# Kernel tuning notes

Measured on AMD Instinct MI355X. Metric: run time of the kernel, lower is better.

Reference implementation:

```python
import jax, jax.numpy as jnp
import numpy as np

VOCAB = 21128
D_WENLAN = 2048
SENT_LEN = 44  # hard-coded in original forward


def setup_inputs() -> dict:
    key = jax.random.key(0)
    ks = jax.random.split(key, 8)
    B, S, P = 32, 8, 32
    L = S * SENT_LEN  # 352
    concat_output = jax.random.normal(ks[0], (B, S, D_WENLAN), jnp.float32)
    input_ids = jax.random.randint(ks[1], (B, L), 0, VOCAB, jnp.int32)
    topic_ids = jax.random.randint(ks[2], (B, P), 0, VOCAB, jnp.int32)
    tpw_att_mask = jnp.ones((B, P), jnp.int32)
    tpw_type_ids = jnp.zeros((B, P), jnp.int32)
    attention_mask = jnp.ones((B, L), jnp.int32)
    type_ids = jax.random.randint(ks[3], (B, L), 0, 8, jnp.int32)
    token_table = jax.random.normal(ks[4], (VOCAB, D_WENLAN), jnp.float32) * 0.02
    W1 = jax.random.normal(ks[5], (D_WENLAN, 512), jnp.float32) * 0.02
    b1 = jnp.zeros((512,), jnp.float32)
    W2 = jax.random.normal(ks[6], (512, 768), jnp.float32) * 0.02
    b2 = jnp.zeros((768,), jnp.float32)
    return dict(concat_output=concat_output, input_ids=input_ids, topic_ids=topic_ids,
                tpw_att_mask=tpw_att_mask, tpw_type_ids=tpw_type_ids,
                attention_mask=attention_mask, type_ids=type_ids,
                token_table=token_table, W1=W1, b1=b1, W2=W2, b2=b2)


def reference(concat_output, input_ids, topic_ids, tpw_att_mask, tpw_type_ids,
              attention_mask, type_ids, token_table, W1, b1, W2, b2):
    B, S, D = concat_output.shape
    # vectorized replacement of the python double-loop dict lookups:
    topic_emb = token_table[topic_ids]                      # [B,P,2048]
    inp_emb = token_table[input_ids]                        # [B,L,2048]
    # scatter-add: each sentence block of 44 tokens gets its concat_output row added
    inp_emb = inp_emb.reshape(B, S, SENT_LEN, D) + concat_output[:, :, None, :]
    input_embs = jnp.concatenate([topic_emb, inp_emb.reshape(B, S * SENT_LEN, D)], axis=1)
    # projector MLP (Linear -> tanh -> Linear)
    h = jnp.tanh(jnp.einsum('btd,dk->btk', input_embs, W1) + b1)
    gpt_input_embs = jnp.einsum('btk,ke->bte', h, W2) + b2   # [B,P+L,768]
    # auxiliary concatenated tensors fed to gpt2 (is_train=True path)
    labels = jnp.concatenate([topic_ids, input_ids], axis=1)
    full_type_ids = jnp.concatenate([tpw_type_ids, type_ids], axis=1)
    full_att_mask = jnp.concatenate([tpw_att_mask, attention_mask], axis=1)
    return gpt_input_embs, labels, full_type_ids, full_att_mask
```

## Files before the change

### kernel.cpp

```cpp
#include <hip/hip_runtime.h>
#include <math.h>

typedef _Float16 half8 __attribute__((ext_vector_type(8)));
typedef float f32x4 __attribute__((ext_vector_type(4)));

#define BB 32
#define SS 8
#define PP 32
#define SENT 44
#define LL 352
#define TT 384
#define DD 2048
#define H1 512
#define H2 768
#define MM (BB*TT)
#define OUT0 (MM*H2)

#define GLL16(g, l) __builtin_amdgcn_global_load_lds( \
    (const __attribute__((address_space(1))) void*)(g), \
    (__attribute__((address_space(3))) void*)(l), 16, 0, 0)

__global__ __launch_bounds__(256) void transpose_f16_kernel(
    const float* __restrict__ src, _Float16* __restrict__ dst, int R, int C)
{
    __shared__ float tile[32][33];
    int c0 = blockIdx.x * 32;
    int r0 = blockIdx.y * 32;
    int tx = threadIdx.x & 31;
    int ty = threadIdx.x >> 5;
    #pragma unroll
    for (int i = 0; i < 4; ++i)
        tile[ty + i*8][tx] = src[(size_t)(r0 + ty + i*8) * C + c0 + tx];
    __syncthreads();
    #pragma unroll
    for (int i = 0; i < 4; ++i)
        dst[(size_t)(c0 + ty + i*8) * R + r0 + tx] = (_Float16)tile[tx][ty + i*8];
}

#define LOADA_T(S, ap, k0) {                                               \
    const float* _p = (ap) + (k0) + akq;                                   \
    float4 v0 = *(const float4*)(_p);                                      \
    float4 v1 = *(const float4*)(_p + 4);                                  \
    float4 v2 = *(const float4*)(_p + 8);                                  \
    float4 v3 = *(const float4*)(_p + 12);                                 \
    S[0]=v0.x; S[1]=v0.y; S[2]=v0.z; S[3]=v0.w;                            \
    S[4]=v1.x; S[5]=v1.y; S[6]=v1.z; S[7]=v1.w;                            \
    S[8]=v2.x; S[9]=v2.y; S[10]=v2.z; S[11]=v2.w;                          \
    S[12]=v3.x; S[13]=v3.y; S[14]=v3.z; S[15]=v3.w;                        \
}

#define WRITEA_T(S, dst) {                                                 \
    half8 h0, h1;                                                          \
    _Pragma("unroll")                                                      \
    for (int _j = 0; _j < 8; ++_j) { h0[_j] = (_Float16)S[_j];             \
                                     h1[_j] = (_Float16)S[8 + _j]; }       \
    *(half8*)&dst[(arow * 64 + akq) ^ aswz]     = h0;                      \
    *(half8*)&dst[(arow * 64 + akq + 8) ^ aswz] = h1;                      \
}

__global__ __launch_bounds__(256) void c1_kernel(
    const float*    __restrict__ concat_output,
    const _Float16* __restrict__ W1T,
    float*          __restrict__ C1)
{
    const int tid  = threadIdx.x;
    const int wid  = tid >> 6;
    const int lane = tid & 63;
    const int bm = blockIdx.x >> 2;
    const int bn = blockIdx.x & 3;

    __shared__ _Float16 As[2][64 * 64];
    __shared__ _Float16 Bs[2][128 * 64];

    const int arow = tid >> 2;
    const int akq  = (tid & 3) * 16;
    const int aswz = (arow & 7) << 3;
    const float* aptr = concat_output + (size_t)(bm * 64 + arow) * DD;

    const int rl = lane >> 3;
    const int cg = lane & 7;
    const _Float16* bsrc = W1T + (size_t)(bn * 128 + wid * 32 + rl) * DD
                               + ((cg ^ rl) << 3);

    #define C1B(buf, k0) {                                                \
        _Pragma("unroll")                                                 \
        for (int q = 0; q < 4; ++q)                                       \
            GLL16(bsrc + (size_t)q * 8 * DD + (k0),                       \
                  &Bs[buf][(wid * 4 + q) * 512]);                         \
    }

    const int wrow = (wid >> 1) * 32;
    const int wcol = (wid & 1) * 64;
    const int fr   = lane & 15;
    const int fg   = lane >> 4;

    f32x4 acc[2][4] = {};
    float a0[16], a1[16];

    C1B(0, 0);
    LOADA_T(a0, aptr, 0);
    LOADA_T(a1, aptr, 64);
    WRITEA_T(a0, As[0]);
    __syncthreads();

    #define C1_MFMA(buf) {                                                \
        _Pragma("unroll")                                                 \
        for (int kk = 0; kk < 2; ++kk) {                                  \
            half8 af[2], bf[4];                                           \
            _Pragma("unroll")                                             \
            for (int i = 0; i < 2; ++i) {                                 \
                int row = wrow + i * 16 + fr;                             \
                af[i] = *(const half8*)&As[buf][                          \
                    (row * 64 + kk * 32 + fg * 8) ^ ((row & 7) << 3)];    \
            }                                                             \
            _Pragma("unroll")                                             \
            for (int j = 0; j < 4; ++j) {                                 \
                int row = wcol + j * 16 + fr;                             \
                bf[j] = *(const half8*)&Bs[buf][                          \
                    (row * 64 + kk * 32 + fg * 8) ^ ((row & 7) << 3)];    \
            }                                                             \
            _Pragma("unroll")                                             \
            for (int i = 0; i < 2; ++i)                                   \
                _Pragma("unroll")                                         \
                for (int j = 0; j < 4; ++j)                               \
                    acc[i][j] = __builtin_amdgcn_mfma_f32_16x16x32_f16(   \
                        af[i], bf[j], acc[i][j], 0, 0, 0);                \
        }                                                                 \
    }

    for (int tt = 0; tt < 16; ++tt) {
        const int t2 = tt * 2;
        C1B(1, (t2 + 1) * 64);
        if (t2 + 2 < 32) LOADA_T(a0, aptr, (t2 + 2) * 64);
        C1_MFMA(0);
        WRITEA_T(a1, As[1]);
        __syncthreads();
        if (t2 + 2 < 32) C1B(0, (t2 + 2) * 64);
        if (t2 + 3 < 32) LOADA_T(a1, aptr, (t2 + 3) * 64);
        C1_MFMA(1);
        if (t2 + 2 < 32) WRITEA_T(a0, As[0]);
        __syncthreads();
    }

    #pragma unroll
    for (int i = 0; i < 2; ++i)
        #pragma unroll
        for (int j = 0; j < 4; ++j) {
            int col = bn * 128 + wcol + j * 16 + fr;
            #pragma unroll
            for (int r = 0; r < 4; ++r) {
                int row = bm * 64 + wrow + i * 16 + fg * 4 + r;
                C1[(size_t)row * H1 + col] = acc[i][j][r];
            }
        }
    #undef C1B
    #undef C1_MFMA
}

__global__ __launch_bounds__(256) void gemm1_kernel(
    const float*    __restrict__ token_table,
    const int*      __restrict__ topic_ids,
    const int*      __restrict__ input_ids,
    const _Float16* __restrict__ W1T,
    const float*    __restrict__ b1,
    const float*    __restrict__ C1,
    _Float16*       __restrict__ Hout)
{
    const int tid  = threadIdx.x;
    const int wid  = tid >> 6;
    const int lane = tid & 63;

    const int logical = ((blockIdx.x & 7) * 96) + (blockIdx.x >> 3);
    const int bm = logical >> 2;
    const int bn = logical & 3;

    __shared__ _Float16 As[2][64 * 64];
    __shared__ _Float16 Bs[2][128 * 64];

    const int arow = tid >> 2;
    const int akq  = (tid & 3) * 16;
    const int aswz = (arow & 7) << 3;

    const int m = bm * 64 + arow;
    const int b = m / TT;
    const int t = m % TT;
    const float* aptr;
    if (t < PP) {
        aptr = token_table + (size_t)topic_ids[b * PP + t] * DD;
    } else {
        aptr = token_table + (size_t)input_ids[b * LL + (t - PP)] * DD;
    }

    const int rl = lane >> 3;
    const int cg = lane & 7;
    const _Float16* bsrc = W1T + (size_t)(bn * 128 + wid * 32 + rl) * DD
                               + ((cg ^ rl) << 3);

    #define G1B(buf, k0) {                                                \
        _Pragma("unroll")                                                 \
        for (int q = 0; q < 4; ++q)                                       \
            GLL16(bsrc + (size_t)q * 8 * DD + (k0),                       \
                  &Bs[buf][(wid * 4 + q) * 512]);                         \
    }

    const int wrow = (wid >> 1) * 32;
    const int wcol = (wid & 1) * 64;
    const int fr   = lane & 15;
    const int fg   = lane >> 4;

    f32x4 acc[2][4] = {};
    float a0[16], a1[16];

    G1B(0, 0);
    LOADA_T(a0, aptr, 0);
    LOADA_T(a1, aptr, 64);
    WRITEA_T(a0, As[0]);
    __syncthreads();

    #define G1_MFMA(buf) {                                                \
        _Pragma("unroll")                                                 \
        for (int kk = 0; kk < 2; ++kk) {                                  \
            half8 af[2], bf[4];                                           \
            _Pragma("unroll")                                             \
            for (int i = 0; i < 2; ++i) {                                 \
                int row = wrow + i * 16 + fr;                             \
                af[i] = *(const half8*)&As[buf][                          \
                    (row * 64 + kk * 32 + fg * 8) ^ ((row & 7) << 3)];    \
            }                                                             \
            _Pragma("unroll")                                             \
            for (int j = 0; j < 4; ++j) {                                 \
                int row = wcol + j * 16 + fr;                             \
                bf[j] = *(const half8*)&Bs[buf][                          \
                    (row * 64 + kk * 32 + fg * 8) ^ ((row & 7) << 3)];    \
            }                                                             \
            _Pragma("unroll")                                             \
            for (int i = 0; i < 2; ++i)                                   \
                _Pragma("unroll")                                         \
                for (int j = 0; j < 4; ++j)                               \
                    acc[i][j] = __builtin_amdgcn_mfma_f32_16x16x32_f16(   \
                        af[i], bf[j], acc[i][j], 0, 0, 0);                \
        }                                                                 \
    }

    for (int tt = 0; tt < 16; ++tt) {
        const int t2 = tt * 2;
        G1B(1, (t2 + 1) * 64);
        if (t2 + 2 < 32) LOADA_T(a0, aptr, (t2 + 2) * 64);
        G1_MFMA(0);
        WRITEA_T(a1, As[1]);
        __syncthreads();
        if (t2 + 2 < 32) G1B(0, (t2 + 2) * 64);
        if (t2 + 3 < 32) LOADA_T(a1, aptr, (t2 + 3) * 64);
        G1_MFMA(1);
        if (t2 + 2 < 32) WRITEA_T(a0, As[0]);
        __syncthreads();
    }

    #pragma unroll
    for (int i = 0; i < 2; ++i) {
        #pragma unroll
        for (int j = 0; j < 4; ++j) {
            int col = bn * 128 + wcol + j * 16 + fr;
            float bias = b1[col];
            #pragma unroll
            for (int r = 0; r < 4; ++r) {
                int row = bm * 64 + wrow + i * 16 + fg * 4 + r;
                int rb = row / TT;
                int rt = row - rb * TT;
                float v = acc[i][j][r] + bias;
                if (rt >= PP)
                    v += C1[(size_t)(rb * SS + (rt - PP) / SENT) * H1 + col];
                Hout[(size_t)row * H1 + col] = (_Float16)tanhf(v);
            }
        }
    }
    #undef G1B
    #undef G1_MFMA
}

__global__ __launch_bounds__(256) void gemm2_kernel(
    const _Float16* __restrict__ Hin,
    const _Float16* __restrict__ W2T,
    const float*    __restrict__ b2,
    float*          __restrict__ out)
{
    const int tid  = threadIdx.x;
    const int wid  = tid >> 6;
    const int lane = tid & 63;

    const int logical = ((blockIdx.x & 7) * 64) + (blockIdx.x >> 3);
    const int bm = logical >> 2;
    const int bn = logical & 3;

    __shared__ _Float16 As[2][96 * 64];
    __shared__ _Float16 Bs[2][192 * 64];

    const int rl = lane >> 3;
    const int cg = lane & 7;
    const _Float16* asrc = Hin + (size_t)(bm * 96 + wid * 24 + rl) * H1
                               + ((cg ^ rl) << 3);
    const _Float16* bsrc = W2T + (size_t)(bn * 192 + wid * 48 + rl) * H1
                               + ((cg ^ rl) << 3);

    #define G2_ISSUE(buf, k0) {                                           \
        _Pragma("unroll")                                                 \
        for (int q = 0; q < 3; ++q)                                       \
            GLL16(asrc + (size_t)q * 8 * H1 + (k0),                       \
                  &As[buf][(wid * 3 + q) * 512]);                         \
        _Pragma("unroll")                                                 \
        for (int q = 0; q < 6; ++q)                                       \
            GLL16(bsrc + (size_t)q * 8 * H1 + (k0),                       \
                  &Bs[buf][(wid * 6 + q) * 512]);                         \
    }

    const int wrow = (wid >> 1) * 48;
    const int wcol = (wid & 1) * 96;
    const int fr   = lane & 15;
    const int fg   = lane >> 4;

    f32x4 acc[3][6] = {};

    G2_ISSUE(0, 0);

    const int NT = H1 / 64;
    for (int t = 0; t < NT; ++t) {
        __syncthreads();
        if (t + 1 < NT) G2_ISSUE((t + 1) & 1, (t + 1) * 64);
        const int cb = t & 1;
        #pragma unroll
        for (int kk = 0; kk < 2; ++kk) {
            half8 af[3], bf[6];
            #pragma unroll
            for (int i = 0; i < 3; ++i) {
                int row = wrow + i * 16 + fr;
                af[i] = *(const half8*)&As[cb][
                    (row * 64 + kk * 32 + fg * 8) ^ ((row & 7) << 3)];
            }
            #pragma unroll
            for (int j = 0; j < 6; ++j) {
                int row = wcol + j * 16 + fr;
                bf[j] = *(const half8*)&Bs[cb][
                    (row * 64 + kk * 32 + fg * 8) ^ ((row & 7) << 3)];
            }
            #pragma unroll
            for (int i = 0; i < 3; ++i)
                #pragma unroll
                for (int j = 0; j < 6; ++j)
                    acc[i][j] = __builtin_amdgcn_mfma_f32_16x16x32_f16(af[i], bf[j], acc[i][j], 0, 0, 0);
        }
    }

    #pragma unroll
    for (int i = 0; i < 3; ++i) {
        #pragma unroll
        for (int j = 0; j < 6; ++j) {
            int col = bn * 192 + wcol + j * 16 + fr;
            float bias = b2[col];
            #pragma unroll
            for (int r = 0; r < 4; ++r) {
                int row = bm * 96 + wrow + i * 16 + fg * 4 + r;
                out[(size_t)row * H2 + col] = acc[i][j][r] + bias;
            }
        }
    }
    #undef G2_ISSUE
}

__global__ __launch_bounds__(256) void aux_kernel(
    const int* __restrict__ topic_ids,
    const int* __restrict__ input_ids,
    const int* __restrict__ tpw_type_ids,
    const int* __restrict__ type_ids,
    const int* __restrict__ tpw_att_mask,
    const int* __restrict__ attention_mask,
    float* __restrict__ out)
{
    int idx = blockIdx.x * 256 + threadIdx.x;
    if (idx >= MM) return;
    int b = idx / TT, t = idx % TT;
    int lab, ty, mk;
    if (t < PP) {
        lab = topic_ids[b * PP + t];
        ty  = tpw_type_ids[b * PP + t];
        mk  = tpw_att_mask[b * PP + t];
    } else {
        int u = t - PP;
        lab = input_ids[b * LL + u];
        ty  = type_ids[b * LL + u];
        mk  = attention_mask[b * LL + u];
    }
    out[OUT0 + idx]          = (float)lab;
    out[OUT0 + MM + idx]     = (float)ty;
    out[OUT0 + 2 * MM + idx] = (float)mk;
}

extern "C" void kernel_launch(void* const* d_in, const int* in_sizes, int n_in,
                              void* d_out, int out_size, void* d_ws, size_t ws_size,
                              hipStream_t stream) {
    const float* concat_output  = (const float*)d_in[0];
    const int*   input_ids      = (const int*)d_in[1];
    const int*   topic_ids      = (const int*)d_in[2];
    const int*   tpw_att_mask   = (const int*)d_in[3];
    const int*   tpw_type_ids   = (const int*)d_in[4];
    const int*   attention_mask = (const int*)d_in[5];
    const int*   type_ids       = (const int*)d_in[6];
    const float* token_table    = (const float*)d_in[7];
    const float* W1             = (const float*)d_in[8];
    const float* b1             = (const float*)d_in[9];
    const float* W2             = (const float*)d_in[10];
    const float* b2             = (const float*)d_in[11];
    float* out = (float*)d_out;

    _Float16* w1t = (_Float16*)d_ws;
    _Float16* w2t = w1t + (size_t)H1 * DD;
    _Float16* Hws = w2t + (size_t)H2 * H1;
    float*    C1w = (float*)(Hws + (size_t)MM * H1);

    transpose_f16_kernel<<<dim3(H1 / 32, DD / 32), 256, 0, stream>>>(W1, w1t, DD, H1);
    transpose_f16_kernel<<<dim3(H2 / 32, H1 / 32), 256, 0, stream>>>(W2, w2t, H1, H2);
    aux_kernel<<<(MM + 255) / 256, 256, 0, stream>>>(
        topic_ids, input_ids, tpw_type_ids, type_ids, tpw_att_mask, attention_mask, out);
    c1_kernel<<<16, 256, 0, stream>>>(concat_output, w1t, C1w);

    gemm1_kernel<<<(MM / 64) * (H1 / 128), 256, 0, stream>>>(
        token_table, topic_ids, input_ids, w1t, b1, C1w, Hws);
    gemm2_kernel<<<(MM / 96) * (H2 / 192), 256, 0, stream>>>(Hws, w2t, b2, out);
}
```

Measured before the change: 110.4 us.

## Retile gemm1 so each block covers full N width, gathering token rows once

The first GEMM now uses 512-thread blocks, each computing a 48-row by 512-column tile with K-steps of 32, instead of 64x128 tiles spread over four column blocks. Each gathered fp32 embedding row is therefore read from the token table and converted once, rather than once per column block, which cuts redundant gather traffic. In exchange there are more K iterations and barriers, 128 of 512 threads sit idle during A loads, and the grid shrinks to 256 blocks, which may underfill the GPU.

```diff
diff --git a/kernel.cpp b/kernel.cpp
--- a/kernel.cpp
+++ b/kernel.cpp
@@ -2,6 +2,7 @@
 #include <math.h>
 
 typedef _Float16 half8 __attribute__((ext_vector_type(8)));
+typedef _Float16 half4v __attribute__((ext_vector_type(4)));
 typedef float f32x4 __attribute__((ext_vector_type(4)));
 
 #define BB 32
@@ -157,7 +158,7 @@
     #undef C1_MFMA
 }
 
-__global__ __launch_bounds__(256) void gemm1_kernel(
+__global__ __launch_bounds__(512) void gemm1_kernel(
     const float*    __restrict__ token_table,
     const int*      __restrict__ topic_ids,
     const int*      __restrict__ input_ids,
@@ -169,102 +170,106 @@
     const int tid  = threadIdx.x;
     const int wid  = tid >> 6;
     const int lane = tid & 63;
-
-    const int logical = ((blockIdx.x & 7) * 96) + (blockIdx.x >> 3);
-    const int bm = logical >> 2;
-    const int bn = logical & 3;
-
-    __shared__ _Float16 As[2][64 * 64];
-    __shared__ _Float16 Bs[2][128 * 64];
-
-    const int arow = tid >> 2;
-    const int akq  = (tid & 3) * 16;
-    const int aswz = (arow & 7) << 3;
-
-    const int m = bm * 64 + arow;
-    const int b = m / TT;
-    const int t = m % TT;
-    const float* aptr;
-    if (t < PP) {
-        aptr = token_table + (size_t)topic_ids[b * PP + t] * DD;
-    } else {
-        aptr = token_table + (size_t)input_ids[b * LL + (t - PP)] * DD;
-    }
-
-    const int rl = lane >> 3;
-    const int cg = lane & 7;
-    const _Float16* bsrc = W1T + (size_t)(bn * 128 + wid * 32 + rl) * DD
-                               + ((cg ^ rl) << 3);
-
-    #define G1B(buf, k0) {                                                \
-        _Pragma("unroll")                                                 \
-        for (int q = 0; q < 4; ++q)                                       \
-            GLL16(bsrc + (size_t)q * 8 * DD + (k0),                       \
-                  &Bs[buf][(wid * 4 + q) * 512]);                         \
-    }
-
-    const int wrow = (wid >> 1) * 32;
-    const int wcol = (wid & 1) * 64;
-    const int fr   = lane & 15;
-    const int fg   = lane >> 4;
-
-    f32x4 acc[2][4] = {};
-    float a0[16], a1[16];
+    const int bm   = blockIdx.x;
+
+    __shared__ _Float16 As[2][48 * 32];
+    __shared__ _Float16 Bs[2][512 * 32];
+
+    const int arow = tid >> 3;
+    const int aseg = tid & 7;
+    const bool aact = tid < 384;
+    const float* aptr = token_table;
+    if (aact) {
+        const int m = bm * 48 + arow;
+        const int b = m / TT;
+        const int t = m % TT;
+        if (t < PP)
+            aptr = token_table + (size_t)topic_ids[b * PP + t] * DD + aseg * 4;
+        else
+            aptr = token_table + (size_t)input_ids[b * LL + (t - PP)] * DD + aseg * 4;
+    }
+    const int awoff = arow * 32 + (((aseg >> 1) ^ (arow & 3)) << 3) + (aseg & 1) * 4;
+
+    #define LOADA(S, k0) { if (aact) {                                     \
+        float4 v = *(const float4*)(aptr + (k0));                          \
+        S[0] = v.x; S[1] = v.y; S[2] = v.z; S[3] = v.w; } }
+
+    #define WRITEA(S, buf) { if (aact) {                                   \
+        half4v h;                                                          \
+        h[0] = (_Float16)S[0]; h[1] = (_Float16)S[1];                      \
+        h[2] = (_Float16)S[2]; h[3] = (_Float16)S[3];                      \
+        *(half4v*)&As[buf][awoff] = h; } }
+
+    const int rl = lane >> 2;
+    const int cg = lane & 3;
+    const _Float16* bsrc = W1T + (size_t)(wid * 64 + rl) * DD
+                               + ((cg ^ (rl & 3)) << 3);
+
+    #define G1B(buf, k0) {                                                 \
+        _Pragma("unroll")                                                  \
+        for (int q = 0; q < 4; ++q)                                        \
+            GLL16(bsrc + (size_t)q * 16 * DD + (k0),                       \
+                  &Bs[buf][(wid * 64 + q * 16) * 32]);                     \
+    }
+
+    const int fr = lane & 15;
+    const int fg = lane >> 4;
+
+    f32x4 acc[3][4] = {};
+
+    #define G1_MFMA(buf) {                                                 \
+        half8 af[3], bf[4];                                                \
+        _Pragma("unroll")                                                  \
+        for (int i = 0; i < 3; ++i) {                                      \
+            int row = i * 16 + fr;                                         \
+            af[i] = *(const half8*)&As[buf][                               \
+                row * 32 + ((fg ^ (row & 3)) << 3)];                       \
+        }                                                                  \
+        _Pragma("unroll")                                                  \
+        for (int j = 0; j < 4; ++j) {                                      \
+            int row = wid * 64 + j * 16 + fr;                              \
+            bf[j] = *(const half8*)&Bs[buf][                               \
+                row * 32 + ((fg ^ (row & 3)) << 3)];                       \
+        }                                                                  \
+        _Pragma("unroll")                                                  \
+        for (int i = 0; i < 3; ++i)                                        \
+            _Pragma("unroll")                                              \
+            for (int j = 0; j < 4; ++j)                                    \
+                acc[i][j] = __builtin_amdgcn_mfma_f32_16x16x32_f16(        \
+                    af[i], bf[j], acc[i][j], 0, 0, 0);                     \
+    }
+
+    float a0[4], a1[4];
 
     G1B(0, 0);
-    LOADA_T(a0, aptr, 0);
-    LOADA_T(a1, aptr, 64);
-    WRITEA_T(a0, As[0]);
+    LOADA(a0, 0);
+    LOADA(a1, 32);
+    WRITEA(a0, 0);
     __syncthreads();
 
-    #define G1_MFMA(buf) {                                                \
-        _Pragma("unroll")                                                 \
-        for (int kk = 0; kk < 2; ++kk) {                                  \
-            half8 af[2], bf[4];                                           \
-            _Pragma("unroll")                                             \
-            for (int i = 0; i < 2; ++i) {                                 \
-                int row = wrow + i * 16 + fr;                             \
-                af[i] = *(const half8*)&As[buf][                          \
-                    (row * 64 + kk * 32 + fg * 8) ^ ((row & 7) << 3)];    \
-            }                                                             \
-            _Pragma("unroll")                                             \
-            for (int j = 0; j < 4; ++j) {                                 \
-                int row = wcol + j * 16 + fr;                             \
-                bf[j] = *(const half8*)&Bs[buf][                          \
-                    (row * 64 + kk * 32 + fg * 8) ^ ((row & 7) << 3)];    \
-            }                                                             \
-            _Pragma("unroll")                                             \
-            for (int i = 0; i < 2; ++i)                                   \
-                _Pragma("unroll")                                         \
-                for (int j = 0; j < 4; ++j)                               \
-                    acc[i][j] = __builtin_amdgcn_mfma_f32_16x16x32_f16(   \
-                        af[i], bf[j], acc[i][j], 0, 0, 0);                \
-        }                                                                 \
-    }
-
-    for (int tt = 0; tt < 16; ++tt) {
+    for (int tt = 0; tt < 32; ++tt) {
         const int t2 = tt * 2;
-        G1B(1, (t2 + 1) * 64);
-        if (t2 + 2 < 32) LOADA_T(a0, aptr, (t2 + 2) * 64);
+        G1B(1, (t2 + 1) * 32);
+        if (t2 + 2 < 64) LOADA(a0, (t2 + 2) * 32);
         G1_MFMA(0);
-        WRITEA_T(a1, As[1]);
+        WRITEA(a1, 1);
         __syncthreads();
-        if (t2 + 2 < 32) G1B(0, (t2 + 2) * 64);
-        if (t2 + 3 < 32) LOADA_T(a1, aptr, (t2 + 3) * 64);
+        if (t2 + 2 < 64) G1B(0, (t2 + 2) * 32);
+        if (t2 + 3 < 64) LOADA(a1, (t2 + 3) * 32);
         G1_MFMA(1);
-        if (t2 + 2 < 32) WRITEA_T(a0, As[0]);
+        if (t2 + 2 < 64) WRITEA(a0, 0);
         __syncthreads();
     }
 
     #pragma unroll
-    for (int i = 0; i < 2; ++i) {
+    for (int i = 0; i < 3; ++i) {
         #pragma unroll
         for (int j = 0; j < 4; ++j) {
-            int col = bn * 128 + wcol + j * 16 + fr;
+            int col = wid * 64 + j * 16 + fr;
             float bias = b1[col];
             #pragma unroll
             for (int r = 0; r < 4; ++r) {
-                int row = bm * 64 + wrow + i * 16 + fg * 4 + r;
+                int row = bm * 48 + i * 16 + fg * 4 + r;
                 int rb = row / TT;
                 int rt = row - rb * TT;
                 float v = acc[i][j][r] + bias;
@@ -274,6 +279,8 @@
             }
         }
     }
+    #undef LOADA
+    #undef WRITEA
     #undef G1B
     #undef G1_MFMA
 }
@@ -302,7 +309,7 @@
     const _Float16* bsrc = W2T + (size_t)(bn * 192 + wid * 48 + rl) * H1
                                + ((cg ^ rl) << 3);
 
-    #define G2_ISSUE(buf, k0) {                                           \
+    #define G2_ISSUE(buf, k0) {                                            \
         _Pragma("unroll")                                                 \
         for (int q = 0; q < 3; ++q)                                       \
             GLL16(asrc + (size_t)q * 8 * H1 + (k0),                       \
@@ -422,7 +429,7 @@
         topic_ids, input_ids, tpw_type_ids, type_ids, tpw_att_mask, attention_mask, out);
     c1_kernel<<<16, 256, 0, stream>>>(concat_output, w1t, C1w);
 
-    gemm1_kernel<<<(MM / 64) * (H1 / 128), 256, 0, stream>>>(
+    gemm1_kernel<<<MM / 48, 512, 0, stream>>>(
         token_table, topic_ids, input_ids, w1t, b1, C1w, Hws);
     gemm2_kernel<<<(MM / 96) * (H2 / 192), 256, 0, stream>>>(Hws, w2t, b2, out);
 }
```

New measurement: 137.6 us. 24.6% more time.

## Retile both GEMMs with async gathered A loads and triple-buffered B pipeline

Applied to the files above, without the earlier changes.

Gemm1 now uses 512-thread blocks with 96x256 tiles, loading gathered fp32 token rows directly into LDS via global_load_lds and converting to fp16 at fragment read, with a triple-buffered W1 tile and explicit waitcnt/barrier scheduling plus setprio around MFMA. Gemm2 is retiled to 128x128 tiles without LDS swizzling. The aim is to overlap the embedding gather with compute and cut register staging. The tradeoffs are heavy LDS use, which limits occupancy, possible bank conflicts in gemm2, and fragile hand-counted vmcnt values.

```diff
diff --git a/kernel.cpp b/kernel.cpp
--- a/kernel.cpp
+++ b/kernel.cpp
@@ -157,7 +157,7 @@
     #undef C1_MFMA
 }
 
-__global__ __launch_bounds__(256) void gemm1_kernel(
+__global__ __launch_bounds__(512) void gemm1_kernel(
     const float*    __restrict__ token_table,
     const int*      __restrict__ topic_ids,
     const int*      __restrict__ input_ids,
@@ -170,101 +170,134 @@
     const int wid  = tid >> 6;
     const int lane = tid & 63;
 
-    const int logical = ((blockIdx.x & 7) * 96) + (blockIdx.x >> 3);
-    const int bm = logical >> 2;
-    const int bn = logical & 3;
-
-    __shared__ _Float16 As[2][64 * 64];
-    __shared__ _Float16 Bs[2][128 * 64];
-
-    const int arow = tid >> 2;
-    const int akq  = (tid & 3) * 16;
-    const int aswz = (arow & 7) << 3;
-
-    const int m = bm * 64 + arow;
-    const int b = m / TT;
-    const int t = m % TT;
-    const float* aptr;
-    if (t < PP) {
-        aptr = token_table + (size_t)topic_ids[b * PP + t] * DD;
-    } else {
-        aptr = token_table + (size_t)input_ids[b * LL + (t - PP)] * DD;
-    }
-
-    const int rl = lane >> 3;
-    const int cg = lane & 7;
-    const _Float16* bsrc = W1T + (size_t)(bn * 128 + wid * 32 + rl) * DD
-                               + ((cg ^ rl) << 3);
-
-    #define G1B(buf, k0) {                                                \
-        _Pragma("unroll")                                                 \
-        for (int q = 0; q < 4; ++q)                                       \
-            GLL16(bsrc + (size_t)q * 8 * DD + (k0),                       \
-                  &Bs[buf][(wid * 4 + q) * 512]);                         \
-    }
-
-    const int wrow = (wid >> 1) * 32;
-    const int wcol = (wid & 1) * 64;
-    const int fr   = lane & 15;
-    const int fg   = lane >> 4;
-
-    f32x4 acc[2][4] = {};
-    float a0[16], a1[16];
-
-    G1B(0, 0);
-    LOADA_T(a0, aptr, 0);
-    LOADA_T(a1, aptr, 64);
-    WRITEA_T(a0, As[0]);
-    __syncthreads();
-
-    #define G1_MFMA(buf) {                                                \
-        _Pragma("unroll")                                                 \
-        for (int kk = 0; kk < 2; ++kk) {                                  \
-            half8 af[2], bf[4];                                           \
-            _Pragma("unroll")                                             \
-            for (int i = 0; i < 2; ++i) {                                 \
-                int row = wrow + i * 16 + fr;                             \
-                af[i] = *(const half8*)&As[buf][                          \
-                    (row * 64 + kk * 32 + fg * 8) ^ ((row & 7) << 3)];    \
-            }                                                             \
-            _Pragma("unroll")                                             \
-            for (int j = 0; j < 4; ++j) {                                 \
-                int row = wcol + j * 16 + fr;                             \
-                bf[j] = *(const half8*)&Bs[buf][                          \
-                    (row * 64 + kk * 32 + fg * 8) ^ ((row & 7) << 3)];    \
-            }                                                             \
-            _Pragma("unroll")                                             \
-            for (int i = 0; i < 2; ++i)                                   \
-                _Pragma("unroll")                                         \
-                for (int j = 0; j < 4; ++j)                               \
-                    acc[i][j] = __builtin_amdgcn_mfma_f32_16x16x32_f16(   \
-                        af[i], bf[j], acc[i][j], 0, 0, 0);                \
-        }                                                                 \
-    }
-
-    for (int tt = 0; tt < 16; ++tt) {
-        const int t2 = tt * 2;
-        G1B(1, (t2 + 1) * 64);
-        if (t2 + 2 < 32) LOADA_T(a0, aptr, (t2 + 2) * 64);
-        G1_MFMA(0);
-        WRITEA_T(a1, As[1]);
-        __syncthreads();
-        if (t2 + 2 < 32) G1B(0, (t2 + 2) * 64);
-        if (t2 + 3 < 32) LOADA_T(a1, aptr, (t2 + 3) * 64);
-        G1_MFMA(1);
-        if (t2 + 2 < 32) WRITEA_T(a0, As[0]);
-        __syncthreads();
-    }
-
-    #pragma unroll
-    for (int i = 0; i < 2; ++i) {
+    const int logical = ((blockIdx.x & 7) * 32) + (blockIdx.x >> 3);
+    const int bm = logical >> 1;
+    const int bn = logical & 1;
+
+    __shared__ float    As[2][96 * 64];
+    __shared__ _Float16 Bs[3][256 * 64];
+
+    const float* asrc[3];
+    #pragma unroll
+    for (int q = 0; q < 3; ++q) {
+        const int ridx = wid * 12 + q * 4 + (lane >> 4);
+        const int m = bm * 96 + ridx;
+        const int b = m / TT;
+        const int t = m % TT;
+        const int id = (t < PP) ? topic_ids[b * PP + t]
+                                : input_ids[b * LL + (t - PP)];
+        asrc[q] = token_table + (size_t)id * DD
+                + (((lane & 15) ^ (ridx & 7)) << 2);
+    }
+    const _Float16* bsrc[4];
+    #pragma unroll
+    for (int q = 0; q < 4; ++q) {
+        const int ridx = wid * 32 + q * 8 + (lane >> 3);
+        bsrc[q] = W1T + (size_t)(bn * 256 + ridx) * DD
+                + (((lane & 7) ^ (ridx & 7)) << 3);
+    }
+
+    #define ISSA(t, slot) {                                                  \
+        _Pragma("unroll")                                                    \
+        for (int q = 0; q < 3; ++q)                                          \
+            GLL16(asrc[q] + (t) * 64, &As[slot][(wid * 12 + q * 4) * 64]);   \
+    }
+    #define ISSB(t, slot) {                                                  \
+        _Pragma("unroll")                                                    \
+        for (int q = 0; q < 4; ++q)                                          \
+            GLL16(bsrc[q] + (t) * 64, &Bs[slot][(wid * 32 + q * 8) * 64]);   \
+    }
+
+    const int wr = wid >> 2;
+    const int wc = wid & 3;
+    const int fr = lane & 15;
+    const int fg = lane >> 4;
+    const int sw = fr & 7;
+
+    f32x4 acc[3][4] = {};
+
+    #define MSTEP(aslot, bslot) {                                            \
+        _Pragma("unroll")                                                    \
+        for (int kk = 0; kk < 2; ++kk) {                                     \
+            half8 af[3], bf[4];                                              \
+            _Pragma("unroll")                                                \
+            for (int i = 0; i < 3; ++i) {                                    \
+                int row = wr * 48 + i * 16 + fr;                             \
+                int g0 = kk * 8 + fg * 2;                                    \
+                f32x4 lo = *(const f32x4*)&As[aslot][row * 64 + ((g0 ^ sw) << 2)];       \
+                f32x4 hi = *(const f32x4*)&As[aslot][row * 64 + (((g0 + 1) ^ sw) << 2)]; \
+                half8 h;                                                     \
+                h[0]=(_Float16)lo[0]; h[1]=(_Float16)lo[1];                  \
+                h[2]=(_Float16)lo[2]; h[3]=(_Float16)lo[3];                  \
+                h[4]=(_Float16)hi[0]; h[5]=(_Float16)hi[1];                  \
+                h[6]=(_Float16)hi[2]; h[7]=(_Float16)hi[3];                  \
+                af[i] = h;                                                   \
+            }                                                                \
+            _Pragma("unroll")                                                \
+            for (int j = 0; j < 4; ++j) {                                    \
+                int row = wc * 64 + j * 16 + fr;                             \
+                int g = kk * 4 + fg;                                         \
+                bf[j] = *(const half8*)&Bs[bslot][row * 64 + ((g ^ sw) << 3)]; \
+            }                                                                \
+            _Pragma("unroll")                                                \
+            for (int i = 0; i < 3; ++i)                                      \
+                _Pragma("unroll")                                            \
+                for (int j = 0; j < 4; ++j)                                  \
+                    acc[i][j] = __builtin_amdgcn_mfma_f32_16x16x32_f16(      \
+                        af[i], bf[j], acc[i][j], 0, 0, 0);                   \
+        }                                                                    \
+    }
+
+    ISSA(0, 0);
+    ISSB(0, 0);
+    ISSB(1, 1);
+
+    for (int t = 0; t < 30; ++t) {
+        __builtin_amdgcn_s_barrier();
+        __builtin_amdgcn_sched_barrier(0);
+        ISSA(t + 1, (t + 1) & 1);
+        ISSB(t + 2, (t + 2) % 3);
+        asm volatile("s_waitcnt vmcnt(11)" ::: "memory");
+        __builtin_amdgcn_sched_barrier(0);
+        __builtin_amdgcn_s_barrier();
+        __builtin_amdgcn_sched_barrier(0);
+        __builtin_amdgcn_s_setprio(1);
+        MSTEP(t & 1, t % 3);
+        __builtin_amdgcn_s_setprio(0);
+    }
+    {
+        __builtin_amdgcn_s_barrier();
+        __builtin_amdgcn_sched_barrier(0);
+        ISSA(31, 1);
+        asm volatile("s_waitcnt vmcnt(7)" ::: "memory");
+        __builtin_amdgcn_sched_barrier(0);
+        __builtin_amdgcn_s_barrier();
+        __builtin_amdgcn_sched_barrier(0);
+        __builtin_amdgcn_s_setprio(1);
+        MSTEP(0, 0);
+        __builtin_amdgcn_s_setprio(0);
+    }
+    {
+        __builtin_amdgcn_s_barrier();
+        __builtin_amdgcn_sched_barrier(0);
+        asm volatile("s_waitcnt vmcnt(0)" ::: "memory");
+        __builtin_amdgcn_sched_barrier(0);
+        __builtin_amdgcn_s_barrier();
+        __builtin_amdgcn_sched_barrier(0);
+        __builtin_amdgcn_s_setprio(1);
+        MSTEP(1, 1);
+        __builtin_amdgcn_s_setprio(0);
+    }
+
+    #pragma unroll
+    for (int i = 0; i < 3; ++i) {
         #pragma unroll
         for (int j = 0; j < 4; ++j) {
-            int col = bn * 128 + wcol + j * 16 + fr;
+            int col = bn * 256 + wc * 64 + j * 16 + fr;
             float bias = b1[col];
             #pragma unroll
             for (int r = 0; r < 4; ++r) {
-                int row = bm * 64 + wrow + i * 16 + fg * 4 + r;
+                int row = bm * 96 + wr * 48 + i * 16 + fg * 4 + r;
                 int rb = row / TT;
                 int rt = row - rb * TT;
                 float v = acc[i][j][r] + bias;
@@ -274,8 +307,9 @@
             }
         }
     }
-    #undef G1B
-    #undef G1_MFMA
+    #undef ISSA
+    #undef ISSB
+    #undef MSTEP
 }
 
 __global__ __launch_bounds__(256) void gemm2_kernel(
@@ -288,37 +322,37 @@
     const int wid  = tid >> 6;
     const int lane = tid & 63;
 
-    const int logical = ((blockIdx.x & 7) * 64) + (blockIdx.x >> 3);
-    const int bm = logical >> 2;
-    const int bn = logical & 3;
-
-    __shared__ _Float16 As[2][96 * 64];
-    __shared__ _Float16 Bs[2][192 * 64];
-
-    const int rl = lane >> 3;
-    const int cg = lane & 7;
-    const _Float16* asrc = Hin + (size_t)(bm * 96 + wid * 24 + rl) * H1
-                               + ((cg ^ rl) << 3);
-    const _Float16* bsrc = W2T + (size_t)(bn * 192 + wid * 48 + rl) * H1
-                               + ((cg ^ rl) << 3);
-
-    #define G2_ISSUE(buf, k0) {                                           \
-        _Pragma("unroll")                                                 \
-        for (int q = 0; q < 3; ++q)                                       \
-            GLL16(asrc + (size_t)q * 8 * H1 + (k0),                       \
-                  &As[buf][(wid * 3 + q) * 512]);                         \
-        _Pragma("unroll")                                                 \
-        for (int q = 0; q < 6; ++q)                                       \
-            GLL16(bsrc + (size_t)q * 8 * H1 + (k0),                       \
-                  &Bs[buf][(wid * 6 + q) * 512]);                         \
-    }
-
-    const int wrow = (wid >> 1) * 48;
-    const int wcol = (wid & 1) * 96;
+    const int logical = ((blockIdx.x & 7) * 72) + (blockIdx.x >> 3);
+    const int bm = logical / 6;
+    const int bn = logical % 6;
+
+    __shared__ _Float16 As[2][128 * 64];
+    __shared__ _Float16 Bs[2][128 * 64];
+
+    const int lrow = lane >> 3;
+    const int lcol = (lane & 7) * 8;
+    const _Float16* ag[4];
+    const _Float16* bg[4];
+    #pragma unroll
+    for (int q = 0; q < 4; ++q) {
+        ag[q] = Hin + (size_t)(bm * 128 + (wid + q * 4) * 8 + lrow) * H1 + lcol;
+        bg[q] = W2T + (size_t)(bn * 128 + (wid + q * 4) * 8 + lrow) * H1 + lcol;
+    }
+
+    #define G2_ISSUE(buf, k0) {                                        \
+        _Pragma("unroll")                                              \
+        for (int q = 0; q < 4; ++q) {                                  \
+            GLL16(ag[q] + (k0), &As[buf][(wid + q * 4) * 512]);        \
+            GLL16(bg[q] + (k0), &Bs[buf][(wid + q * 4) * 512]);        \
+        }                                                              \
+    }
+
+    const int wrow = (wid >> 1) * 64;
+    const int wcol = (wid & 1) * 64;
     const int fr   = lane & 15;
     const int fg   = lane >> 4;
 
-    f32x4 acc[3][6] = {};
+    f32x4 acc[4][4] = {};
 
     G2_ISSUE(0, 0);
 
@@ -329,36 +363,30 @@
         const int cb = t & 1;
         #pragma unroll
         for (int kk = 0; kk < 2; ++kk) {
-            half8 af[3], bf[6];
-            #pragma unroll
-            for (int i = 0; i < 3; ++i) {
-                int row = wrow + i * 16 + fr;
-                af[i] = *(const half8*)&As[cb][
-                    (row * 64 + kk * 32 + fg * 8) ^ ((row & 7) << 3)];
-            }
-            #pragma unroll
-            for (int j = 0; j < 6; ++j) {
-                int row = wcol + j * 16 + fr;
-                bf[j] = *(const half8*)&Bs[cb][
-                    (row * 64 + kk * 32 + fg * 8) ^ ((row & 7) << 3)];
-            }
-            #pragma unroll
-            for (int i = 0; i < 3; ++i)
+            half8 af[4], bf[4];
+            #pragma unroll
+            for (int i = 0; i < 4; ++i)
+                af[i] = *(const half8*)&As[cb][(wrow + i*16 + fr) * 64 + kk*32 + fg*8];
+            #pragma unroll
+            for (int j = 0; j < 4; ++j)
+                bf[j] = *(const half8*)&Bs[cb][(wcol + j*16 + fr) * 64 + kk*32 + fg*8];
+            #pragma unroll
+            for (int i = 0; i < 4; ++i)
                 #pragma unroll
-                for (int j = 0; j < 6; ++j)
+                for (int j = 0; j < 4; ++j)
                     acc[i][j] = __builtin_amdgcn_mfma_f32_16x16x32_f16(af[i], bf[j], acc[i][j], 0, 0, 0);
         }
     }
 
     #pragma unroll
-    for (int i = 0; i < 3; ++i) {
+    for (int i = 0; i < 4; ++i) {
         #pragma unroll
-        for (int j = 0; j < 6; ++j) {
-            int col = bn * 192 + wcol + j * 16 + fr;
+        for (int j = 0; j < 4; ++j) {
+            int col = bn * 128 + wcol + j * 16 + fr;
             float bias = b2[col];
             #pragma unroll
             for (int r = 0; r < 4; ++r) {
-                int row = bm * 96 + wrow + i * 16 + fg * 4 + r;
+                int row = bm * 128 + wrow + i * 16 + fg * 4 + r;
                 out[(size_t)row * H2 + col] = acc[i][j][r] + bias;
             }
         }
@@ -422,7 +450,7 @@
         topic_ids, input_ids, tpw_type_ids, type_ids, tpw_att_mask, attention_mask, out);
     c1_kernel<<<16, 256, 0, stream>>>(concat_output, w1t, C1w);
 
-    gemm1_kernel<<<(MM / 64) * (H1 / 128), 256, 0, stream>>>(
+    gemm1_kernel<<<(MM / 96) * 2, 512, 0, stream>>>(
         token_table, topic_ids, input_ids, w1t, b1, C1w, Hws);
-    gemm2_kernel<<<(MM / 96) * (H2 / 192), 256, 0, stream>>>(Hws, w2t, b2, out);
-}
+    gemm2_kernel<<<(MM / 128) * (H2 / 128), 256, 0, stream>>>(Hws, w2t, b2, out);
+}
```

Measured after the change: 130.4 us. 1.18x slower.

## Retile gemm1 to 48x256 blocks to cut redundant gathered-row loads

Applied to the files above, without the earlier changes.

Gemm1 now uses 48-row by 256-column tiles instead of 64x128. Each gathered token_table row is loaded by only two blocks instead of four, which halves the fp32 gather traffic for A, the dominant memory cost. In exchange, a quarter of the threads sit idle during A loads, B tile traffic per block doubles, and the block count falls from 768 to 512. Each wave now covers all 48 rows by 64 columns.

```diff
diff --git a/kernel.cpp b/kernel.cpp
--- a/kernel.cpp
+++ b/kernel.cpp
@@ -170,60 +170,56 @@
     const int wid  = tid >> 6;
     const int lane = tid & 63;
 
-    const int logical = ((blockIdx.x & 7) * 96) + (blockIdx.x >> 3);
-    const int bm = logical >> 2;
-    const int bn = logical & 3;
-
-    __shared__ _Float16 As[2][64 * 64];
-    __shared__ _Float16 Bs[2][128 * 64];
+    const int logical = ((blockIdx.x & 7) * 64) + (blockIdx.x >> 3);
+    const int bm = logical >> 1;
+    const int bn = logical & 1;
+
+    __shared__ _Float16 As[2][48 * 64];
+    __shared__ _Float16 Bs[2][256 * 64];
 
     const int arow = tid >> 2;
     const int akq  = (tid & 3) * 16;
     const int aswz = (arow & 7) << 3;
-
-    const int m = bm * 64 + arow;
-    const int b = m / TT;
-    const int t = m % TT;
-    const float* aptr;
-    if (t < PP) {
-        aptr = token_table + (size_t)topic_ids[b * PP + t] * DD;
-    } else {
-        aptr = token_table + (size_t)input_ids[b * LL + (t - PP)] * DD;
+    const bool aact = tid < 192;
+
+    const float* aptr = token_table;
+    if (aact) {
+        const int m = bm * 48 + arow;
+        const int b = m / TT;
+        const int t = m % TT;
+        const int id = (t < PP) ? topic_ids[b * PP + t]
+                                : input_ids[b * LL + (t - PP)];
+        aptr = token_table + (size_t)id * DD;
     }
 
     const int rl = lane >> 3;
     const int cg = lane & 7;
-    const _Float16* bsrc = W1T + (size_t)(bn * 128 + wid * 32 + rl) * DD
+    const _Float16* bsrc = W1T + (size_t)(bn * 256 + wid * 64 + rl) * DD
                                + ((cg ^ rl) << 3);
 
     #define G1B(buf, k0) {                                                \
         _Pragma("unroll")                                                 \
-        for (int q = 0; q < 4; ++q)                                       \
+        for (int q = 0; q < 8; ++q)                                       \
             GLL16(bsrc + (size_t)q * 8 * DD + (k0),                       \
-                  &Bs[buf][(wid * 4 + q) * 512]);                         \
-    }
-
-    const int wrow = (wid >> 1) * 32;
-    const int wcol = (wid & 1) * 64;
+                  &Bs[buf][(wid * 64 + q * 8) * 64]);                     \
+    }
+
+    #define LOADA(S, k0) { if (aact) LOADA_T(S, aptr, k0) }
+    #define WRITEA(S, buf) { if (aact) WRITEA_T(S, As[buf]) }
+
+    const int wcol = wid * 64;
     const int fr   = lane & 15;
     const int fg   = lane >> 4;
 
-    f32x4 acc[2][4] = {};
-    float a0[16], a1[16];
-
-    G1B(0, 0);
-    LOADA_T(a0, aptr, 0);
-    LOADA_T(a1, aptr, 64);
-    WRITEA_T(a0, As[0]);
-    __syncthreads();
+    f32x4 acc[3][4] = {};
 
     #define G1_MFMA(buf) {                                                \
         _Pragma("unroll")                                                 \
         for (int kk = 0; kk < 2; ++kk) {                                  \
-            half8 af[2], bf[4];                                           \
-            _Pragma("unroll")                                             \
-            for (int i = 0; i < 2; ++i) {                                 \
-                int row = wrow + i * 16 + fr;                             \
+            half8 af[3], bf[4];                                           \
+            _Pragma("unroll")                                             \
+            for (int i = 0; i < 3; ++i) {                                 \
+                int row = i * 16 + fr;                                    \
                 af[i] = *(const half8*)&As[buf][                          \
                     (row * 64 + kk * 32 + fg * 8) ^ ((row & 7) << 3)];    \
             }                                                             \
@@ -234,7 +230,7 @@
                     (row * 64 + kk * 32 + fg * 8) ^ ((row & 7) << 3)];    \
             }                                                             \
             _Pragma("unroll")                                             \
-            for (int i = 0; i < 2; ++i)                                   \
+            for (int i = 0; i < 3; ++i)                                   \
                 _Pragma("unroll")                                         \
                 for (int j = 0; j < 4; ++j)                               \
                     acc[i][j] = __builtin_amdgcn_mfma_f32_16x16x32_f16(   \
@@ -242,29 +238,37 @@
         }                                                                 \
     }
 
+    float a0[16], a1[16];
+
+    G1B(0, 0);
+    LOADA(a0, 0);
+    LOADA(a1, 64);
+    WRITEA(a0, 0);
+    __syncthreads();
+
     for (int tt = 0; tt < 16; ++tt) {
         const int t2 = tt * 2;
         G1B(1, (t2 + 1) * 64);
-        if (t2 + 2 < 32) LOADA_T(a0, aptr, (t2 + 2) * 64);
+        if (t2 + 2 < 32) LOADA(a0, (t2 + 2) * 64);
         G1_MFMA(0);
-        WRITEA_T(a1, As[1]);
+        WRITEA(a1, 1);
         __syncthreads();
         if (t2 + 2 < 32) G1B(0, (t2 + 2) * 64);
-        if (t2 + 3 < 32) LOADA_T(a1, aptr, (t2 + 3) * 64);
+        if (t2 + 3 < 32) LOADA(a1, (t2 + 3) * 64);
         G1_MFMA(1);
-        if (t2 + 2 < 32) WRITEA_T(a0, As[0]);
+        if (t2 + 2 < 32) WRITEA(a0, 0);
         __syncthreads();
     }
 
     #pragma unroll
-    for (int i = 0; i < 2; ++i) {
+    for (int i = 0; i < 3; ++i) {
         #pragma unroll
         for (int j = 0; j < 4; ++j) {
-            int col = bn * 128 + wcol + j * 16 + fr;
+            int col = bn * 256 + wcol + j * 16 + fr;
             float bias = b1[col];
             #pragma unroll
             for (int r = 0; r < 4; ++r) {
-                int row = bm * 64 + wrow + i * 16 + fg * 4 + r;
+                int row = bm * 48 + i * 16 + fg * 4 + r;
                 int rb = row / TT;
                 int rt = row - rb * TT;
                 float v = acc[i][j][r] + bias;
@@ -275,6 +279,8 @@
         }
     }
     #undef G1B
+    #undef LOADA
+    #undef WRITEA
     #undef G1_MFMA
 }
 
@@ -422,7 +428,7 @@
         topic_ids, input_ids, tpw_type_ids, type_ids, tpw_att_mask, attention_mask, out);
     c1_kernel<<<16, 256, 0, stream>>>(concat_output, w1t, C1w);
 
-    gemm1_kernel<<<(MM / 64) * (H1 / 128), 256, 0, stream>>>(
+    gemm1_kernel<<<(MM / 48) * 2, 256, 0, stream>>>(
         token_table, topic_ids, input_ids, w1t, b1, C1w, Hws);
     gemm2_kernel<<<(MM / 96) * (H2 / 192), 256, 0, stream>>>(Hws, w2t, b2, out);
 }
```

Result: no change. 110.5 us (+0.1%).
